# Kernel tuning notes

Hardware: AMD Instinct MI355X
Metric: run time of the kernel (lower is better)

## Reference

```python
import jax, jax.numpy as jnp
import numpy as np

N_WIN = 8  # matches init kwarg n_win

def setup_inputs() -> dict:
    key = jax.random.key(0)
    k1, k2, k3 = jax.random.split(key, 3)
    c = 64
    x = jax.random.normal(k1, (1, c, 256, 256), dtype=jnp.float32)
    W = jax.random.normal(k2, (3 * c, c), dtype=jnp.float32) * 0.05
    bias = jax.random.normal(k3, (3 * c,), dtype=jnp.float32) * 0.05
    return {"x": x, "W": W, "bias": bias}

def reference(x, W, bias):
    b, c, h, w = x.shape
    n_h = n_w = N_WIN
    hs, ws = h // n_h, w // n_w
    nw = n_h * n_w
    # unfold into non-overlapping windows: [1, nw, hs*ws, c]
    xw = x.reshape(b, c, n_h, hs, n_w, ws)
    xw = xw.transpose(0, 2, 4, 3, 5, 1).reshape(1, nw, hs * ws, c)
    # shared QKV linear
    qkv = xw @ W.T + bias
    q, k, v = qkv[..., :c], qkv[..., c:2 * c], qkv[..., 2 * c:3 * c]
    # region-level routing via mean-pooled tokens
    q_r = q.mean(axis=2)  # [1, nw, c]
    k_r = k.mean(axis=2)
    a_r = jax.nn.relu(jnp.einsum('bic,bjc->bij', q_r, k_r))  # [1, nw, nw]
    # mix windows: a_r @ flattened(k/q) == window-mixing einsum
    k_m = jnp.einsum('bij,bjtc->bitc', a_r, k)
    q_m = jnp.einsum('bij,bjtc->bitc', a_r, q)
    # relu-gated windowed attention
    attn = jax.nn.relu(jnp.einsum('bitc,bisc->bits', q_m, k_m))  # [1, nw, T, T]
    o = jnp.einsum('bits,bisc->bitc', attn, v)  # [1, nw, T, c]
    # fold back to image
    o = o.reshape(b, n_h, n_w, hs, ws, c).transpose(0, 5, 1, 3, 2, 4).reshape(b, c, h, w)
    return o
```

## Files before the change

### kernel.cpp

```cpp
#include <hip/hip_runtime.h>

typedef _Float16 half_t;
typedef __attribute__((ext_vector_type(8))) _Float16 half8;
typedef __attribute__((ext_vector_type(4))) _Float16 half4;
typedef __attribute__((ext_vector_type(4))) float floatx4;
typedef __attribute__((ext_vector_type(16))) float floatx16;

#define MFMA16(A, B, C) __builtin_amdgcn_mfma_f32_16x16x32_f16((A), (B), (C), 0, 0, 0)
#define MFMA32(A, B, C) __builtin_amdgcn_mfma_f32_32x32x16_f16((A), (B), (C), 0, 0, 0)

__global__ __launch_bounds__(256) void k_qkv(
    const float* __restrict__ x, const float* __restrict__ W,
    const float* __restrict__ bias, half_t* __restrict__ q,
    half_t* __restrict__ k, half_t* __restrict__ vT,
    float* __restrict__ qp, float* __restrict__ kp) {
  __shared__ __align__(16) char smem[52736];
  half_t(*Xs)[72] = (half_t(*)[72])smem;
  half_t(*Ws)[72] = (half_t(*)[72])(smem + 18432);
  half_t(*S1)[136] = (half_t(*)[136])smem;
  half_t(*S2)[136] = (half_t(*)[136])(smem + 34816);
  float* qs_l = (float*)(smem + 52224);
  float* ks_l = qs_l + 64;
  const int w = blockIdx.y;
  const int tx = blockIdx.x;
  const int t0 = tx * 128;
  const int ih = w >> 3, iw = w & 7;
  const int xbase = ih * 8192 + iw * 32;
  const int tid = threadIdx.x;

  for (int i = tid; i < 8192; i += 256) {
    const int c = i >> 7, tt = i & 127;
    const int t = t0 + tt;
    Xs[tt][c] = (half_t)x[c * 65536 + xbase + (t >> 5) * 256 + (t & 31)];
  }
  for (int i = tid; i < 3072; i += 256) {
    const int o = i >> 4, c4 = (i & 15) * 4;
    const floatx4 v = *(const floatx4*)&W[o * 64 + c4];
    half4 hv;
    #pragma unroll
    for (int p = 0; p < 4; p++) hv[p] = (half_t)v[p];
    *(half4*)&Ws[o][c4] = hv;
  }
  if (tid < 64) { qs_l[tid] = 0.f; ks_l[tid] = 0.f; }
  __syncthreads();

  const int wave = tid >> 6, lane = tid & 63;
  const int lrow = lane & 15, lq = lane >> 4;
  const int rbase = (wave >> 1) * 64;
  const int cbase = (wave & 1) * 96;

  floatx4 acc[4][6];
  const floatx4 z = {0.f, 0.f, 0.f, 0.f};
  #pragma unroll
  for (int mt = 0; mt < 4; mt++)
    #pragma unroll
    for (int nt = 0; nt < 6; nt++) acc[mt][nt] = z;

  #pragma unroll
  for (int kf = 0; kf < 2; kf++) {
    const int koff = kf * 32 + lq * 8;
    half8 a[4], b[6];
    #pragma unroll
    for (int mt = 0; mt < 4; mt++)
      a[mt] = *(const half8*)&Xs[rbase + mt * 16 + lrow][koff];
    #pragma unroll
    for (int nt = 0; nt < 6; nt++)
      b[nt] = *(const half8*)&Ws[cbase + nt * 16 + lrow][koff];
    #pragma unroll
    for (int mt = 0; mt < 4; mt++)
      #pragma unroll
      for (int nt = 0; nt < 6; nt++)
        acc[mt][nt] = MFMA16(a[mt], b[nt], acc[mt][nt]);
  }
  __syncthreads();

  #pragma unroll
  for (int nt = 0; nt < 6; nt++) {
    const int o = cbase + nt * 16 + lrow;
    const float bs = bias[o];
    if (o < 128) {
      float s = 0.f;
      #pragma unroll
      for (int mt = 0; mt < 4; mt++) {
        const int tr = rbase + mt * 16 + lq * 4;
        #pragma unroll
        for (int r = 0; r < 4; r++) {
          const float v = acc[mt][nt][r] + bs;
          S1[tr + r][o] = (half_t)v;
          s += v;
        }
      }
      if (o < 64) atomicAdd(&qs_l[o], s);
      else atomicAdd(&ks_l[o - 64], s);
    } else {
      const int oc = o - 128;
      #pragma unroll
      for (int mt = 0; mt < 4; mt++) {
        const int tr = rbase + mt * 16 + lq * 4;
        half4 pk;
        #pragma unroll
        for (int r = 0; r < 4; r++) pk[r] = (half_t)(acc[mt][nt][r] + bs);
        *(half4*)&S2[oc][tr] = pk;
      }
    }
  }
  __syncthreads();

  for (int idx = tid; idx < 3072; idx += 256) {
    if (idx < 2048) {
      const int t = idx >> 4, seg = idx & 15;
      const half8 v = *(const half8*)&S1[t][seg * 8];
      if (seg < 8)
        *(half8*)&q[w * 65536 + (t0 + t) * 64 + seg * 8] = v;
      else
        *(half8*)&k[w * 65536 + (t0 + t) * 64 + (seg - 8) * 8] = v;
    } else {
      const int i2 = idx - 2048;
      const int oc = i2 >> 4, seg = i2 & 15;
      *(half8*)&vT[w * 65536 + oc * 1024 + t0 + seg * 8] =
          *(const half8*)&S2[oc][seg * 8];
    }
  }
  if (tid < 64) {
    qp[(w * 8 + tx) * 64 + tid] = qs_l[tid];
    kp[(w * 8 + tx) * 64 + tid] = ks_l[tid];
  }
}

__global__ __launch_bounds__(256) void k_mix(const half_t* __restrict__ q,
                                             const half_t* __restrict__ k,
                                             const float* __restrict__ qp,
                                             const float* __restrict__ kp,
                                             half_t* __restrict__ qm,
                                             half_t* __restrict__ km) {
  __shared__ __align__(16) half_t qh[64][72];
  __shared__ __align__(16) half_t kh[64][72];
  __shared__ __align__(16) half_t arL[64][72];
  const half_t* __restrict__ src = blockIdx.y ? k : q;
  half_t* __restrict__ dst = blockIdx.y ? km : qm;
  const int tid = threadIdx.x;
  const int wave = tid >> 6, lane = tid & 63;
  const int ln31 = lane & 31;
  const int hk8 = (lane >> 5) * 8;
  const int lrow = lane & 15, lq = lane >> 4;

  const int pos0 = blockIdx.x * 256 + wave * 64 + ln31;
  half8 bB0[4];
  #pragma unroll
  for (int kk = 0; kk < 4; kk++)
    #pragma unroll
    for (int jj = 0; jj < 8; jj++)
      bB0[kk][jj] = src[(kk * 16 + hk8 + jj) * 65536 + pos0];

  for (int e = tid; e < 1024; e += 256) {
    const int i = e >> 4, c4 = (e & 15) * 4;
    floatx4 sq = {0.f, 0.f, 0.f, 0.f}, sk = {0.f, 0.f, 0.f, 0.f};
    #pragma unroll
    for (int t = 0; t < 8; t++) {
      sq += *(const floatx4*)&qp[i * 512 + t * 64 + c4];
      sk += *(const floatx4*)&kp[i * 512 + t * 64 + c4];
    }
    #pragma unroll
    for (int p = 0; p < 4; p++) {
      qh[i][c4 + p] = (half_t)sq[p];
      kh[i][c4 + p] = (half_t)sk[p];
    }
  }
  __syncthreads();

  {
    floatx4 ac[4];
    const floatx4 z = {0.f, 0.f, 0.f, 0.f};
    #pragma unroll
    for (int nt = 0; nt < 4; nt++) ac[nt] = z;
    #pragma unroll
    for (int kf = 0; kf < 2; kf++) {
      const int koff = kf * 32 + lq * 8;
      const half8 aF = *(const half8*)&qh[wave * 16 + lrow][koff];
      #pragma unroll
      for (int nt = 0; nt < 4; nt++) {
        const half8 bF = *(const half8*)&kh[nt * 16 + lrow][koff];
        ac[nt] = MFMA16(aF, bF, ac[nt]);
      }
    }
    const float scale = 1.f / (1024.f * 1024.f);
    #pragma unroll
    for (int nt = 0; nt < 4; nt++)
      #pragma unroll
      for (int r = 0; r < 4; r++) {
        const float v = ac[nt][r] * scale;
        arL[wave * 16 + lq * 4 + r][nt * 16 + lrow] = (half_t)(v > 0.f ? v : 0.f);
      }
  }
  __syncthreads();

  half8 aA[2][4];
  #pragma unroll
  for (int mt = 0; mt < 2; mt++)
    #pragma unroll
    for (int kk = 0; kk < 4; kk++)
      aA[mt][kk] = *(const half8*)&arL[mt * 32 + ln31][kk * 16 + hk8];

  #pragma unroll
  for (int t32 = 0; t32 < 2; t32++) {
    const int pos = blockIdx.x * 256 + wave * 64 + t32 * 32 + ln31;
    half8 bB[4];
    if (t32 == 0) {
      #pragma unroll
      for (int kk = 0; kk < 4; kk++) bB[kk] = bB0[kk];
    } else {
      #pragma unroll
      for (int kk = 0; kk < 4; kk++)
        #pragma unroll
        for (int jj = 0; jj < 8; jj++)
          bB[kk][jj] = src[(kk * 16 + hk8 + jj) * 65536 + pos];
    }

    floatx16 c0, c1;
    #pragma unroll
    for (int r = 0; r < 16; r++) { c0[r] = 0.f; c1[r] = 0.f; }
    #pragma unroll
    for (int kk = 0; kk < 4; kk++) {
      c0 = MFMA32(aA[0][kk], bB[kk], c0);
      c1 = MFMA32(aA[1][kk], bB[kk], c1);
    }
    const int h4 = (lane >> 5) * 4;
    #pragma unroll
    for (int r = 0; r < 16; r++) {
      const int row = (r & 3) + h4 + 8 * (r >> 2);
      dst[row * 65536 + pos] = (half_t)c0[r];
      dst[(32 + row) * 65536 + pos] = (half_t)c1[r];
    }
  }
}

__global__ __launch_bounds__(256, 2) void k_attn(const half_t* __restrict__ qm,
                                                 const half_t* __restrict__ km,
                                                 const half_t* __restrict__ vT,
                                                 float* __restrict__ out) {
  __shared__ __align__(16) half_t Vs[64][136];
  __shared__ __align__(16) half_t St[128][138];
  const int w = blockIdx.x;
  const int t0 = blockIdx.y * 128;
  const int tid = threadIdx.x;
  const int wave = tid >> 6, lane = tid & 63;
  const int ln31 = lane & 31;
  const int hk8 = (lane >> 5) * 8, hk4 = (lane >> 5) * 4;
  const int w32 = wave * 32;
  const int wbase = w * 65536;

  half8 bQ[4][4];
  #pragma unroll
  for (int tt = 0; tt < 4; tt++)
    #pragma unroll
    for (int kk = 0; kk < 4; kk++)
      bQ[tt][kk] = *(const half8*)&qm[wbase + (t0 + tt * 32 + ln31) * 64 + kk * 16 + hk8];

  floatx16 oacc[2];
  #pragma unroll
  for (int ct = 0; ct < 2; ct++)
    #pragma unroll
    for (int r = 0; r < 16; r++) oacc[ct][r] = 0.f;

  for (int sc = 0; sc < 8; sc++) {
    const int s0 = sc * 128;
    __syncthreads();
    for (int idx = tid; idx < 1024; idx += 256) {
      const int c = idx >> 4, so = (idx & 15) * 8;
      *(half8*)&Vs[c][so] = *(const half8*)&vT[wbase + c * 1024 + s0 + so];
    }
    half8 aK[4];
    #pragma unroll
    for (int kk = 0; kk < 4; kk++)
      aK[kk] = *(const half8*)&km[wbase + (s0 + w32 + ln31) * 64 + kk * 16 + hk8];
    __syncthreads();

    floatx16 sacc[4];
    #pragma unroll
    for (int tt = 0; tt < 4; tt++)
      #pragma unroll
      for (int r = 0; r < 16; r++) sacc[tt][r] = 0.f;
    #pragma unroll
    for (int kk = 0; kk < 4; kk++)
      #pragma unroll
      for (int tt = 0; tt < 4; tt++)
        sacc[tt] = MFMA32(aK[kk], bQ[tt][kk], sacc[tt]);

    #pragma unroll
    for (int tt = 0; tt < 4; tt++) {
      const int t = tt * 32 + ln31;
      #pragma unroll
      for (int g = 0; g < 4; g++) {
        const int s = w32 + g * 8 + hk4;
        half4 pk;
        #pragma unroll
        for (int p = 0; p < 4; p++) {
          const float v = sacc[tt][g * 4 + p];
          pk[p] = (half_t)(v > 0.f ? v : 0.f);
        }
        *(half4*)&St[t][s] = pk;
      }
    }
    __syncthreads();

    #pragma unroll
    for (int kk = 0; kk < 8; kk++) {
      const half8 bS = *(const half8*)&St[w32 + ln31][kk * 16 + hk8];
      #pragma unroll
      for (int ct = 0; ct < 2; ct++) {
        const half8 aV = *(const half8*)&Vs[ct * 32 + ln31][kk * 16 + hk8];
        oacc[ct] = MFMA32(aV, bS, oacc[ct]);
      }
    }
  }

  const int ih = w >> 3, iw = w & 7;
  const int obase = ih * 8192 + iw * 32;
  const int tb = ((t0 + w32) >> 5) * 256 + ln31;
  const int h4 = (lane >> 5) * 4;
  #pragma unroll
  for (int ct = 0; ct < 2; ct++) {
    #pragma unroll
    for (int r = 0; r < 16; r++) {
      const int c = ct * 32 + (r & 3) + h4 + 8 * (r >> 2);
      out[c * 65536 + obase + tb] = oacc[ct][r];
    }
  }
}

extern "C" void kernel_launch(void* const* d_in, const int* in_sizes, int n_in,
                              void* d_out, int out_size, void* d_ws, size_t ws_size,
                              hipStream_t stream) {
  const float* x = (const float*)d_in[0];
  const float* W = (const float*)d_in[1];
  const float* bias = (const float*)d_in[2];
  float* out = (float*)d_out;

  half_t* q = (half_t*)d_ws;
  half_t* k = q + 4194304;
  half_t* vT = k + 4194304;
  half_t* qm = vT + 4194304;
  half_t* km = qm + 4194304;
  float* qp = (float*)(km + 4194304);
  float* kp = qp + 32768;

  k_qkv<<<dim3(8, 64), 256, 0, stream>>>(x, W, bias, q, k, vT, qp, kp);
  k_mix<<<dim3(256, 2), 256, 0, stream>>>(q, k, qp, kp, qm, km);
  k_attn<<<dim3(64, 8), 256, 0, stream>>>(qm, km, vT, out);
}
```

Before: 124.0 us.

## Prefetch next V/K chunk in attention, vectorize x load, atomic-reduce pooled sums

The attention kernel now prefetches the next chunk's V and K tiles into registers while the current chunk's QK MFMAs and relu/store run. This removes one barrier per iteration and hides global load latency, and s_setprio raises wave priority around the MFMA blocks. The QKV kernel loads x with float4 vectors instead of scalar gathers. Per-tile pooled sums are atomically accumulated into per-window buffers, so the mix kernel reads one vector instead of summing eight, at the cost of an extra memset launch and float atomics.

```diff
diff --git a/kernel.cpp b/kernel.cpp
--- a/kernel.cpp
+++ b/kernel.cpp
@@ -13,7 +13,7 @@
     const float* __restrict__ x, const float* __restrict__ W,
     const float* __restrict__ bias, half_t* __restrict__ q,
     half_t* __restrict__ k, half_t* __restrict__ vT,
-    float* __restrict__ qp, float* __restrict__ kp) {
+    float* __restrict__ qsum, float* __restrict__ ksum) {
   __shared__ __align__(16) char smem[52736];
   half_t(*Xs)[72] = (half_t(*)[72])smem;
   half_t(*Ws)[72] = (half_t(*)[72])(smem + 18432);
@@ -25,13 +25,16 @@
   const int tx = blockIdx.x;
   const int t0 = tx * 128;
   const int ih = w >> 3, iw = w & 7;
-  const int xbase = ih * 8192 + iw * 32;
+  const int xbase = ih * 8192 + iw * 32 + tx * 1024;
   const int tid = threadIdx.x;
 
-  for (int i = tid; i < 8192; i += 256) {
-    const int c = i >> 7, tt = i & 127;
-    const int t = t0 + tt;
-    Xs[tt][c] = (half_t)x[c * 65536 + xbase + (t >> 5) * 256 + (t & 31)];
+  for (int i = tid; i < 2048; i += 256) {
+    const int c = i >> 5, g = i & 31;
+    const int tt = (g >> 3) * 32 + (g & 7) * 4;
+    const floatx4 v =
+        *(const floatx4*)&x[c * 65536 + xbase + (g >> 3) * 256 + (g & 7) * 4];
+    #pragma unroll
+    for (int p = 0; p < 4; p++) Xs[tt + p][c] = (half_t)v[p];
   }
   for (int i = tid; i < 3072; i += 256) {
     const int o = i >> 4, c4 = (i & 15) * 4;
@@ -122,15 +125,15 @@
     }
   }
   if (tid < 64) {
-    qp[(w * 8 + tx) * 64 + tid] = qs_l[tid];
-    kp[(w * 8 + tx) * 64 + tid] = ks_l[tid];
+    atomicAdd(&qsum[w * 64 + tid], qs_l[tid]);
+    atomicAdd(&ksum[w * 64 + tid], ks_l[tid]);
   }
 }
 
 __global__ __launch_bounds__(256) void k_mix(const half_t* __restrict__ q,
                                              const half_t* __restrict__ k,
-                                             const float* __restrict__ qp,
-                                             const float* __restrict__ kp,
+                                             const float* __restrict__ qsum,
+                                             const float* __restrict__ ksum,
                                              half_t* __restrict__ qm,
                                              half_t* __restrict__ km) {
   __shared__ __align__(16) half_t qh[64][72];
@@ -154,12 +157,8 @@
 
   for (int e = tid; e < 1024; e += 256) {
     const int i = e >> 4, c4 = (e & 15) * 4;
-    floatx4 sq = {0.f, 0.f, 0.f, 0.f}, sk = {0.f, 0.f, 0.f, 0.f};
-    #pragma unroll
-    for (int t = 0; t < 8; t++) {
-      sq += *(const floatx4*)&qp[i * 512 + t * 64 + c4];
-      sk += *(const floatx4*)&kp[i * 512 + t * 64 + c4];
-    }
+    const floatx4 sq = *(const floatx4*)&qsum[i * 64 + c4];
+    const floatx4 sk = *(const floatx4*)&ksum[i * 64 + c4];
     #pragma unroll
     for (int p = 0; p < 4; p++) {
       qh[i][c4 + p] = (half_t)sq[p];
@@ -189,7 +188,8 @@
       #pragma unroll
       for (int r = 0; r < 4; r++) {
         const float v = ac[nt][r] * scale;
-        arL[wave * 16 + lq * 4 + r][nt * 16 + lrow] = (half_t)(v > 0.f ? v : 0.f);
+        arL[wave * 16 + lq * 4 + r][nt * 16 + lrow] =
+            (half_t)(v > 0.f ? v : 0.f);
       }
   }
   __syncthreads();
@@ -254,7 +254,8 @@
   for (int tt = 0; tt < 4; tt++)
     #pragma unroll
     for (int kk = 0; kk < 4; kk++)
-      bQ[tt][kk] = *(const half8*)&qm[wbase + (t0 + tt * 32 + ln31) * 64 + kk * 16 + hk8];
+      bQ[tt][kk] = *(const half8*)&qm[wbase + (t0 + tt * 32 + ln31) * 64 +
+                                      kk * 16 + hk8];
 
   floatx16 oacc[2];
   #pragma unroll
@@ -262,30 +263,39 @@
     #pragma unroll
     for (int r = 0; r < 16; r++) oacc[ct][r] = 0.f;
 
+  half8 vpre[4], aK[4];
+  #pragma unroll
+  for (int j = 0; j < 4; j++) {
+    const int idx = j * 256 + tid;
+    const int c = idx >> 4, so = (idx & 15) * 8;
+    vpre[j] = *(const half8*)&vT[wbase + c * 1024 + so];
+  }
+  #pragma unroll
+  for (int kk = 0; kk < 4; kk++)
+    aK[kk] = *(const half8*)&km[wbase + (w32 + ln31) * 64 + kk * 16 + hk8];
+
   for (int sc = 0; sc < 8; sc++) {
-    const int s0 = sc * 128;
-    __syncthreads();
-    for (int idx = tid; idx < 1024; idx += 256) {
-      const int c = idx >> 4, so = (idx & 15) * 8;
-      *(half8*)&Vs[c][so] = *(const half8*)&vT[wbase + c * 1024 + s0 + so];
-    }
-    half8 aK[4];
-    #pragma unroll
-    for (int kk = 0; kk < 4; kk++)
-      aK[kk] = *(const half8*)&km[wbase + (s0 + w32 + ln31) * 64 + kk * 16 + hk8];
-    __syncthreads();
-
     floatx16 sacc[4];
     #pragma unroll
     for (int tt = 0; tt < 4; tt++)
       #pragma unroll
       for (int r = 0; r < 16; r++) sacc[tt][r] = 0.f;
+    __builtin_amdgcn_s_setprio(1);
     #pragma unroll
     for (int kk = 0; kk < 4; kk++)
       #pragma unroll
       for (int tt = 0; tt < 4; tt++)
         sacc[tt] = MFMA32(aK[kk], bQ[tt][kk], sacc[tt]);
-
+    __builtin_amdgcn_s_setprio(0);
+
+    __syncthreads();
+
+    #pragma unroll
+    for (int j = 0; j < 4; j++) {
+      const int idx = j * 256 + tid;
+      const int c = idx >> 4, so = (idx & 15) * 8;
+      *(half8*)&Vs[c][so] = vpre[j];
+    }
     #pragma unroll
     for (int tt = 0; tt < 4; tt++) {
       const int t = tt * 32 + ln31;
@@ -301,8 +311,23 @@
         *(half4*)&St[t][s] = pk;
       }
     }
+    half8 aKn[4];
+    if (sc < 7) {
+      const int s0n = (sc + 1) * 128;
+      #pragma unroll
+      for (int j = 0; j < 4; j++) {
+        const int idx = j * 256 + tid;
+        const int c = idx >> 4, so = (idx & 15) * 8;
+        vpre[j] = *(const half8*)&vT[wbase + c * 1024 + s0n + so];
+      }
+      #pragma unroll
+      for (int kk = 0; kk < 4; kk++)
+        aKn[kk] = *(const half8*)&km[wbase + (s0n + w32 + ln31) * 64 +
+                                     kk * 16 + hk8];
+    }
     __syncthreads();
 
+    __builtin_amdgcn_s_setprio(1);
     #pragma unroll
     for (int kk = 0; kk < 8; kk++) {
       const half8 bS = *(const half8*)&St[w32 + ln31][kk * 16 + hk8];
@@ -311,6 +336,11 @@
         const half8 aV = *(const half8*)&Vs[ct * 32 + ln31][kk * 16 + hk8];
         oacc[ct] = MFMA32(aV, bS, oacc[ct]);
       }
+    }
+    __builtin_amdgcn_s_setprio(0);
+    if (sc < 7) {
+      #pragma unroll
+      for (int kk = 0; kk < 4; kk++) aK[kk] = aKn[kk];
     }
   }
 
@@ -341,10 +371,11 @@
   half_t* vT = k + 4194304;
   half_t* qm = vT + 4194304;
   half_t* km = qm + 4194304;
-  float* qp = (float*)(km + 4194304);
-  float* kp = qp + 32768;
-
-  k_qkv<<<dim3(8, 64), 256, 0, stream>>>(x, W, bias, q, k, vT, qp, kp);
-  k_mix<<<dim3(256, 2), 256, 0, stream>>>(q, k, qp, kp, qm, km);
+  float* qsum = (float*)(km + 4194304);
+  float* ksum = qsum + 4096;
+
+  hipMemsetAsync(qsum, 0, 2 * 4096 * sizeof(float), stream);
+  k_qkv<<<dim3(8, 64), 256, 0, stream>>>(x, W, bias, q, k, vT, qsum, ksum);
+  k_mix<<<dim3(256, 2), 256, 0, stream>>>(q, k, qsum, ksum, qm, km);
   k_attn<<<dim3(64, 8), 256, 0, stream>>>(qm, km, vT, out);
 }
```

Measured after the change: 115.8 us. 6.6% less time.
